# Kernel tuning notes

Measured on AMD Instinct MI355X. Metric: run time of the kernel, lower is better.

## Reference

```python
import jax, jax.numpy as jnp
import numpy as np

K = 16  # neighbors

def setup_inputs() -> dict:
    key = jax.random.key(0)
    x = jax.random.normal(key, (2, 8192, 64), dtype=jnp.float32)
    return {"x": x}

def reference(x):
    # pairwise squared euclidean distance: ||xi||^2 - 2 xi.xj + ||xj||^2
    b, n, d = x.shape
    x_inner = -2.0 * jnp.einsum('bnd,bmd->bnm', x, x)          # (B,N,N)
    x_sq = jnp.sum(x * x, axis=-1, keepdims=True)               # (B,N,1)
    dist = x_sq + x_inner + jnp.swapaxes(x_sq, 1, 2)            # (B,N,N)
    # torch.topk(-dist, k) -> largest of -dist == k nearest neighbors
    _, nn_idx = jax.lax.top_k(-dist, K)                         # (B,N,K) int32
    center_idx = jnp.broadcast_to(jnp.arange(n, dtype=nn_idx.dtype)[None, :, None], (b, n, K))
    return jnp.stack((nn_idx, center_idx), axis=0)              # (2,B,N,K)
```

## Files before the change

### kernel.cpp

```cpp
#include <hip/hip_runtime.h>
#include <stdint.h>

constexpr int N_   = 8192;
constexpr int D_   = 64;
constexpr int K_   = 16;
constexpr int NQ   = 16384;
constexpr int MS   = 8;
constexpr int CAPB = 32;
constexpr float SLOP = 0.012f;

typedef __attribute__((ext_vector_type(8))) short bf16x8;
typedef __attribute__((ext_vector_type(4))) float f32x4;

template<int JN>
__device__ __forceinline__ void topk_insertf(float (&key)[JN], float nk) {
    if (nk < key[JN - 1]) {
        bool c[JN];
#pragma unroll
        for (int j = 0; j < JN; ++j) c[j] = nk < key[j];
#pragma unroll
        for (int j = JN - 1; j >= 1; --j)
            key[j] = c[j - 1] ? key[j - 1] : (c[j] ? nk : key[j]);
        key[0] = c[0] ? nk : key[0];
    }
}

__device__ __forceinline__ unsigned short bf16_rne(float f) {
    uint32_t u = __float_as_uint(f);
    return (unsigned short)((u + 0x7FFFu + ((u >> 16) & 1u)) >> 16);
}

__device__ __forceinline__ void gl_lds16(const void* g, void* l) {
    __builtin_amdgcn_global_load_lds(
        (const __attribute__((address_space(1))) unsigned int*)g,
        (__attribute__((address_space(3))) unsigned int*)l, 16, 0, 0);
}

#define SWZ(r, s) (((r) << 7) + ((((s) ^ ((r) & 7))) << 4))

__global__ void __launch_bounds__(256) split_k(const float* __restrict__ x,
                                               unsigned short* __restrict__ xh,
                                               unsigned short* __restrict__ xl,
                                               float* __restrict__ nrm) {
    const int t = blockIdx.x * 256 + (int)threadIdx.x;
    const int row = t >> 4, seg = t & 15;
    const float4 v = reinterpret_cast<const float4*>(x)[t];
    float f[4] = {v.x, v.y, v.z, v.w};
    unsigned short h[4], l[4];
    float sq = 0.f;
#pragma unroll
    for (int j = 0; j < 4; ++j) {
        sq = fmaf(f[j], f[j], sq);
        h[j] = bf16_rne(f[j]);
        float hf = __uint_as_float((uint32_t)h[j] << 16);
        l[j] = bf16_rne(f[j] - hf);
    }
    sq += __shfl_xor(sq, 1, 16); sq += __shfl_xor(sq, 2, 16);
    sq += __shfl_xor(sq, 4, 16); sq += __shfl_xor(sq, 8, 16);
    if (seg == 0) nrm[row] = sq;
    ushort4 hv = {h[0], h[1], h[2], h[3]}, lv = {l[0], l[1], l[2], l[3]};
    reinterpret_cast<ushort4*>(xh)[t] = hv;
    reinterpret_cast<ushort4*>(xl)[t] = lv;
}

__global__ void __launch_bounds__(256) tau_p(const unsigned short* __restrict__ xh,
                                             const unsigned short* __restrict__ xl,
                                             const float* __restrict__ nrm,
                                             float* __restrict__ part) {
    __shared__ alignas(16) unsigned short A[64 * 64];
    __shared__ alignas(16) unsigned short Bb[256 * 64];
    __shared__ float nrmb[128];
    const int tid = (int)threadIdx.x;
    const int q0g = (int)blockIdx.x * 32;
    const int b   = q0g >> 13;
    const int n0  = q0g & (N_ - 1);
    const unsigned short* __restrict__ xhb = xh + (size_t)b * N_ * D_;
    const unsigned short* __restrict__ xlb = xl + (size_t)b * N_ * D_;
    const float* __restrict__ nb = nrm + b * N_;

#pragma unroll
    for (int k = 0; k < 2; ++k) {
        int u = tid + k * 256, r = u >> 3, s = u & 7;
        const unsigned short* src = (r < 32) ? xhb + (size_t)(n0 + r) * D_
                                             : xlb + (size_t)(n0 + r - 32) * D_;
        *(float4*)((char*)A + SWZ(r, s)) = *(const float4*)((const char*)src + (s << 4));
    }

    const int wave = tid >> 6, lane = tid & 63;
    const int l15 = lane & 15, quad = lane >> 4;

    float lad0[8], lad1[8];
#pragma unroll
    for (int j = 0; j < 8; ++j) { lad0[j] = __builtin_inff(); lad1[j] = __builtin_inff(); }

    for (int mc = 0; mc < 16; ++mc) {
        const int m0 = mc * 128;
        __syncthreads();
#pragma unroll
        for (int k = 0; k < 8; ++k) {
            int u = tid + k * 256, r = u >> 3, s = u & 7;
            const unsigned short* src = (r < 128) ? xhb + (size_t)(m0 + r) * D_
                                                  : xlb + (size_t)(m0 + r - 128) * D_;
            *(float4*)((char*)Bb + SWZ(r, s)) = *(const float4*)((const char*)src + (s << 4));
        }
        if (tid < 128) nrmb[tid] = nb[m0 + tid];
        __syncthreads();

        f32x4 acc[2][2] = {};
#pragma unroll
        for (int half = 0; half < 2; ++half) {
            const int seg = half * 4 + quad;
            bf16x8 afh[2], afl[2], bfh[2], bfl[2];
#pragma unroll
            for (int tm = 0; tm < 2; ++tm) {
                afh[tm] = *(const bf16x8*)((const char*)A + SWZ(tm * 16 + l15, seg));
                afl[tm] = *(const bf16x8*)((const char*)A + SWZ(32 + tm * 16 + l15, seg));
            }
#pragma unroll
            for (int tn = 0; tn < 2; ++tn) {
                bfh[tn] = *(const bf16x8*)((const char*)Bb + SWZ(wave * 32 + tn * 16 + l15, seg));
                bfl[tn] = *(const bf16x8*)((const char*)Bb + SWZ(128 + wave * 32 + tn * 16 + l15, seg));
            }
#pragma unroll
            for (int tm = 0; tm < 2; ++tm)
#pragma unroll
                for (int tn = 0; tn < 2; ++tn) {
                    acc[tm][tn] = __builtin_amdgcn_mfma_f32_16x16x32_bf16(afh[tm], bfh[tn], acc[tm][tn], 0, 0, 0);
                    acc[tm][tn] = __builtin_amdgcn_mfma_f32_16x16x32_bf16(afh[tm], bfl[tn], acc[tm][tn], 0, 0, 0);
                    acc[tm][tn] = __builtin_amdgcn_mfma_f32_16x16x32_bf16(afl[tm], bfh[tn], acc[tm][tn], 0, 0, 0);
                }
        }
#pragma unroll
        for (int tn = 0; tn < 2; ++tn) {
            const float nm = nrmb[wave * 32 + tn * 16 + l15];
#pragma unroll
            for (int tm = 0; tm < 2; ++tm)
#pragma unroll
                for (int reg = 0; reg < 4; ++reg) {
                    float keyf = fmaf(-2.f, acc[tm][tn][reg], nm);
                    const int li = tm * 4 + reg;
                    float k0 = lad0[li];
                    lad0[li] = fminf(k0, keyf);
                    lad1[li] = fminf(fmaxf(keyf, k0), lad1[li]);
                }
        }
    }
#pragma unroll
    for (int tm = 0; tm < 2; ++tm)
#pragma unroll
        for (int reg = 0; reg < 4; ++reg) {
            const int r = tm * 16 + quad * 4 + reg;
            const int li = tm * 4 + reg;
            float2 v = {lad0[li], lad1[li]};
            *(float2*)(part + ((size_t)(q0g + r)) * 128 + (wave * 16 + l15) * 2) = v;
        }
}

__global__ void __launch_bounds__(64) tau_m(const float* __restrict__ part,
                                            float* __restrict__ tau) {
    const int q = blockIdx.x * 64 + (int)threadIdx.x;
    const float4* p = reinterpret_cast<const float4*>(part + (size_t)q * 128);
    float key[K_];
#pragma unroll
    for (int j = 0; j < K_; ++j) key[j] = __builtin_inff();
    for (int i = 0; i < 32; ++i) {
        float4 v = p[i];
        topk_insertf<K_>(key, v.x); topk_insertf<K_>(key, v.y);
        topk_insertf<K_>(key, v.z); topk_insertf<K_>(key, v.w);
    }
    tau[q] = key[15] + SLOP;
}

__global__ void __launch_bounds__(256, 2) filter_k(const unsigned short* __restrict__ xh,
                                                   const unsigned short* __restrict__ xl,
                                                   const float* __restrict__ nrm,
                                                   const float* __restrict__ tau,
                                                   unsigned short* __restrict__ cnt_pb,
                                                   unsigned short* __restrict__ buf2) {
    __shared__ alignas(16) unsigned short A[256 * 64];
    __shared__ alignas(16) unsigned short Bd[2][128 * 64];
    __shared__ alignas(16) float taub[128];
    __shared__ alignas(16) float nrmS[1024];
    __shared__ unsigned short lists[128 * CAPB];
    __shared__ unsigned int cntL[128];
    const int tid = (int)threadIdx.x;
    const int bid = (int)blockIdx.x;
    const int b  = bid >> 9;
    const int qt = (bid >> 3) & 63;
    const int ms = bid & 7;
    const int q0 = qt * 128;
    const unsigned short* __restrict__ xhb = xh + (size_t)b * N_ * D_;
    const unsigned short* __restrict__ xlb = xl + (size_t)b * N_ * D_;
    const float* __restrict__ nb = nrm + b * N_;
    const int w = tid >> 6;

#pragma unroll
    for (int k = 0; k < 8; ++k) {
        int u = k * 256 + tid, r = u >> 3, sg = (u & 7) ^ (r & 7);
        const unsigned short* src = (r < 128) ? xhb + (size_t)(q0 + r) * D_
                                              : xlb + (size_t)(q0 + r - 128) * D_;
        gl_lds16((const char*)src + (sg << 4), (char*)A + (k << 12) + (w << 10));
    }
    {
        const int m0 = ms * 1024;
#pragma unroll
        for (int k = 0; k < 4; ++k) {
            int u = k * 256 + tid, r = u >> 3, sg = (u & 7) ^ (r & 7);
            const unsigned short* src = (r < 64) ? xhb + (size_t)(m0 + r) * D_
                                                 : xlb + (size_t)(m0 + r - 64) * D_;
            gl_lds16((const char*)src + (sg << 4), (char*)Bd[0] + (k << 12) + (w << 10));
        }
    }
    *(float4*)(nrmS + tid * 4) = *(const float4*)(nb + ms * 1024 + tid * 4);
    if (tid < 128) { cntL[tid] = 0; taub[tid] = tau[(b << 13) + q0 + tid]; }
    __syncthreads();

    const int lane = tid & 63;
    const int wq = w >> 1, wm = w & 1;
    const int l15 = lane & 15, quad = lane >> 4;

    bf16x8 Afh[2][4], Afl[2][4];
#pragma unroll
    for (int half = 0; half < 2; ++half) {
        const int seg = half * 4 + quad;
#pragma unroll
        for (int tm = 0; tm < 4; ++tm) {
            Afh[half][tm] = *(const bf16x8*)((const char*)A + SWZ(wq * 64 + tm * 16 + l15, seg));
            Afl[half][tm] = *(const bf16x8*)((const char*)A + SWZ(128 + wq * 64 + tm * 16 + l15, seg));
        }
    }
    f32x4 t4v[4];
#pragma unroll
    for (int tm = 0; tm < 4; ++tm)
        t4v[tm] = *(const f32x4*)(taub + wq * 64 + tm * 16 + quad * 4) + SLOP;

    for (int mc = 0; mc < 16; ++mc) {
        const int cur = mc & 1;
        if (mc < 15) {
            const int m0n = ms * 1024 + (mc + 1) * 64;
#pragma unroll
            for (int k = 0; k < 4; ++k) {
                int u = k * 256 + tid, r = u >> 3, sg = (u & 7) ^ (r & 7);
                const unsigned short* src = (r < 64) ? xhb + (size_t)(m0n + r) * D_
                                                     : xlb + (size_t)(m0n + r - 64) * D_;
                gl_lds16((const char*)src + (sg << 4), (char*)Bd[1 - cur] + (k << 12) + (w << 10));
            }
        }

        f32x4 acc[4][2] = {};
#pragma unroll
        for (int half = 0; half < 2; ++half) {
            const int seg = half * 4 + quad;
            bf16x8 bfh[2], bfl[2];
#pragma unroll
            for (int tn = 0; tn < 2; ++tn) {
                bfh[tn] = *(const bf16x8*)((const char*)Bd[cur] + SWZ(wm * 32 + tn * 16 + l15, seg));
                bfl[tn] = *(const bf16x8*)((const char*)Bd[cur] + SWZ(64 + wm * 32 + tn * 16 + l15, seg));
            }
#pragma unroll
            for (int tm = 0; tm < 4; ++tm)
#pragma unroll
                for (int tn = 0; tn < 2; ++tn) {
                    acc[tm][tn] = __builtin_amdgcn_mfma_f32_16x16x32_bf16(Afh[half][tm], bfh[tn], acc[tm][tn], 0, 0, 0);
                    acc[tm][tn] = __builtin_amdgcn_mfma_f32_16x16x32_bf16(Afh[half][tm], bfl[tn], acc[tm][tn], 0, 0, 0);
                    acc[tm][tn] = __builtin_amdgcn_mfma_f32_16x16x32_bf16(Afl[half][tm], bfh[tn], acc[tm][tn], 0, 0, 0);
                }
        }

        float nmv[2]; int mlv[2];
#pragma unroll
        for (int tn = 0; tn < 2; ++tn) {
            mlv[tn] = mc * 64 + wm * 32 + tn * 16 + l15;
            nmv[tn] = nrmS[mlv[tn]];
        }
#pragma unroll
        for (int tm = 0; tm < 4; ++tm)
#pragma unroll
            for (int tn = 0; tn < 2; ++tn)
#pragma unroll
                for (int reg = 0; reg < 4; ++reg) {
                    float keyf = fmaf(-2.f, acc[tm][tn][reg], nmv[tn]);
                    if (keyf <= t4v[tm][reg]) {
                        int ql = wq * 64 + tm * 16 + quad * 4 + reg;
                        unsigned pos = atomicAdd(&cntL[ql], 1u);
                        if (pos < CAPB) lists[ql * CAPB + pos] = (unsigned short)(ms * 1024 + mlv[tn]);
                    }
                }

        __syncthreads();
    }
    if (tid < 128) {
        int q = (b << 13) + q0 + tid;
        unsigned cn = cntL[tid]; cn = cn < CAPB ? cn : CAPB;
        cnt_pb[(size_t)q * MS + ms] = (unsigned short)cn;
        unsigned short* dst = buf2 + ((size_t)q * MS + ms) * CAPB;
        for (unsigned i = 0; i < cn; ++i) dst[i] = lists[tid * CAPB + i];
    }
}

__global__ void __launch_bounds__(256) rerank_k(const float* __restrict__ x,
                                                const unsigned short* __restrict__ cnt_pb,
                                                const unsigned short* __restrict__ buf2,
                                                int* __restrict__ out) {
    __shared__ float Qs[4 * 64];
    __shared__ unsigned short ids[4 * MS * CAPB];
    const int tid = (int)threadIdx.x;
    const int w = tid >> 6, lane = tid & 63;
    const int q = blockIdx.x * 4 + w;
    const int b = q >> 13, n = q & (N_ - 1);
    const float* __restrict__ xb = x + (size_t)b * N_ * D_;
    Qs[w * 64 + lane] = xb[(size_t)n * D_ + lane];

    int off[MS + 1]; off[0] = 0;
#pragma unroll
    for (int ms = 0; ms < MS; ++ms) {
        int c = (int)cnt_pb[(size_t)q * MS + ms]; c = c < CAPB ? c : CAPB;
        off[ms + 1] = off[ms] + c;
    }
    const int total = off[MS];
    for (int idx = lane; idx < total; idx += 64) {
        int ms = 0;
#pragma unroll
        for (int t = 1; t < MS; ++t) ms += (idx >= off[t]) ? 1 : 0;
        ids[(w * MS) * CAPB + idx] = buf2[((size_t)q * MS + ms) * CAPB + (idx - off[ms])];
    }
    __syncthreads();

    unsigned long long v = ~0ull;
    int consumed = 0;
    bool first = true;
    while (first || consumed < total) {
        const int myIdx = first ? lane : consumed + lane - 16;
        const bool take = (first || lane >= 16) && myIdx < total;
        unsigned long long nk = ~0ull;
        if (take) {
            const int id = (int)ids[(w * MS) * CAPB + myIdx];
            const float* __restrict__ crow = xb + (size_t)id * D_;
            double a0 = 0.0, a1 = 0.0, a2 = 0.0, a3 = 0.0;
#pragma unroll
            for (int j = 0; j < 16; ++j) {
                const float4 c  = *(const float4*)(crow + j * 4);
                const float4 qv = *(const float4*)(Qs + w * 64 + j * 4);
                double d0 = (double)qv.x - (double)c.x; a0 = fma(d0, d0, a0);
                double d1 = (double)qv.y - (double)c.y; a1 = fma(d1, d1, a1);
                double d2 = (double)qv.z - (double)c.z; a2 = fma(d2, d2, a2);
                double d3 = (double)qv.w - (double)c.w; a3 = fma(d3, d3, a3);
            }
            double s = (a0 + a1) + (a2 + a3);
            nk = ((unsigned long long)__double_as_longlong(s) & ~0x1FFFull) | (unsigned)id;
        }
        if (first || lane >= 16) v = nk;
#pragma unroll
        for (int k = 2; k <= 64; k <<= 1)
#pragma unroll
            for (int j = k >> 1; j > 0; j >>= 1) {
                unsigned long long o = __shfl_xor(v, j, 64);
                const bool keepmin = (((lane & k) == 0) == ((lane & j) == 0));
                unsigned long long mn = v < o ? v : o;
                unsigned long long mx = v < o ? o : v;
                v = keepmin ? mn : mx;
            }
        consumed += first ? 64 : 48;
        first = false;
    }
    if (lane < K_) {
        out[(size_t)q * K_ + lane]                   = (int)(v & 0x1FFFull);
        out[(size_t)NQ * K_ + (size_t)q * K_ + lane] = n;
    }
}

extern "C" void kernel_launch(void* const* d_in, const int* in_sizes, int n_in,
                              void* d_out, int out_size, void* d_ws, size_t ws_size,
                              hipStream_t stream) {
    const float* x = (const float*)d_in[0];
    int* out = (int*)d_out;
    char* ws = (char*)d_ws;
    float*          nrm    = (float*)ws;
    float*          tau    = (float*)(ws + (64 << 10));
    unsigned short* cnt_pb = (unsigned short*)(ws + (128 << 10));
    unsigned short* xh     = (unsigned short*)(ws + (1 << 20));
    unsigned short* xl     = (unsigned short*)(ws + (3 << 20));
    unsigned short* buf2   = (unsigned short*)(ws + (5 << 20));
    float*          part   = (float*)(ws + (5 << 20));

    hipLaunchKernelGGL(split_k,  dim3(1024), dim3(256), 0, stream, x, xh, xl, nrm);
    hipLaunchKernelGGL(tau_p,    dim3(512),  dim3(256), 0, stream, xh, xl, nrm, part);
    hipLaunchKernelGGL(tau_m,    dim3(256),  dim3(64),  0, stream, part, tau);
    hipLaunchKernelGGL(filter_k, dim3(1024), dim3(256), 0, stream, xh, xl, nrm, tau, cnt_pb, buf2);
    hipLaunchKernelGGL(rerank_k, dim3(4096), dim3(256), 0, stream, x, cnt_pb, buf2, out);
}
```

Baseline: 242.5 us.

## Keep query fragments in registers, ballot-compact filter lists, and split tau_p across shards

Result: slower. 267.8 us (+10.4%).

```diff
diff --git a/kernel.cpp b/kernel.cpp
--- a/kernel.cpp
+++ b/kernel.cpp
@@ -1,12 +1,13 @@
 #include <hip/hip_runtime.h>
 #include <stdint.h>
 
-constexpr int N_   = 8192;
-constexpr int D_   = 64;
-constexpr int K_   = 16;
-constexpr int NQ   = 16384;
-constexpr int MS   = 8;
-constexpr int CAPB = 32;
+constexpr int N_    = 8192;
+constexpr int D_    = 64;
+constexpr int K_    = 16;
+constexpr int NQ    = 16384;
+constexpr int MS    = 8;
+constexpr int CAP_H = 20;
+constexpr int CAPB  = 2 * CAP_H;
 constexpr float SLOP = 0.012f;
 
 typedef __attribute__((ext_vector_type(8))) short bf16x8;
@@ -63,96 +64,102 @@
     reinterpret_cast<ushort4*>(xl)[t] = lv;
 }
 
-__global__ void __launch_bounds__(256) tau_p(const unsigned short* __restrict__ xh,
-                                             const unsigned short* __restrict__ xl,
-                                             const float* __restrict__ nrm,
-                                             float* __restrict__ part) {
-    __shared__ alignas(16) unsigned short A[64 * 64];
-    __shared__ alignas(16) unsigned short Bb[256 * 64];
-    __shared__ float nrmb[128];
+__global__ void __launch_bounds__(256, 4) tau_p(const unsigned short* __restrict__ xh,
+                                                const unsigned short* __restrict__ xl,
+                                                const float* __restrict__ nrm,
+                                                float* __restrict__ part) {
+    __shared__ alignas(16) unsigned short Bd[2][128 * 64];
+    __shared__ alignas(16) float nrmS[512];
     const int tid = (int)threadIdx.x;
-    const int q0g = (int)blockIdx.x * 32;
+    const int bid = (int)blockIdx.x;
+    const int qb  = bid >> 2, sh = bid & 3;
+    const int q0g = qb * 64;
     const int b   = q0g >> 13;
-    const int n0  = q0g & (N_ - 1);
+    const int q0l = q0g & (N_ - 1);
+    const int s0  = sh * 512;
     const unsigned short* __restrict__ xhb = xh + (size_t)b * N_ * D_;
     const unsigned short* __restrict__ xlb = xl + (size_t)b * N_ * D_;
     const float* __restrict__ nb = nrm + b * N_;
-
-#pragma unroll
-    for (int k = 0; k < 2; ++k) {
-        int u = tid + k * 256, r = u >> 3, s = u & 7;
-        const unsigned short* src = (r < 32) ? xhb + (size_t)(n0 + r) * D_
-                                             : xlb + (size_t)(n0 + r - 32) * D_;
-        *(float4*)((char*)A + SWZ(r, s)) = *(const float4*)((const char*)src + (s << 4));
-    }
-
-    const int wave = tid >> 6, lane = tid & 63;
+    const int w = tid >> 6, lane = tid & 63;
+    const int wq = w >> 1, wm = w & 1;
     const int l15 = lane & 15, quad = lane >> 4;
 
-    float lad0[8], lad1[8];
-#pragma unroll
-    for (int j = 0; j < 8; ++j) { lad0[j] = __builtin_inff(); lad1[j] = __builtin_inff(); }
-
-    for (int mc = 0; mc < 16; ++mc) {
-        const int m0 = mc * 128;
-        __syncthreads();
-#pragma unroll
-        for (int k = 0; k < 8; ++k) {
-            int u = tid + k * 256, r = u >> 3, s = u & 7;
-            const unsigned short* src = (r < 128) ? xhb + (size_t)(m0 + r) * D_
-                                                  : xlb + (size_t)(m0 + r - 128) * D_;
-            *(float4*)((char*)Bb + SWZ(r, s)) = *(const float4*)((const char*)src + (s << 4));
-        }
-        if (tid < 128) nrmb[tid] = nb[m0 + tid];
-        __syncthreads();
-
+    bf16x8 Afh[2][2], Afl[2][2];
+#pragma unroll
+    for (int half = 0; half < 2; ++half) {
+        const int ko = (half * 4 + quad) << 4;
+#pragma unroll
+        for (int tm = 0; tm < 2; ++tm) {
+            const int r = q0l + wq * 32 + tm * 16 + l15;
+            Afh[half][tm] = *(const bf16x8*)((const char*)(xhb + (size_t)r * D_) + ko);
+            Afl[half][tm] = *(const bf16x8*)((const char*)(xlb + (size_t)r * D_) + ko);
+        }
+    }
+    {
+#pragma unroll
+        for (int k = 0; k < 4; ++k) {
+            int u = k * 256 + tid, r = u >> 3, sg = (u & 7) ^ (r & 7);
+            const unsigned short* src = (r < 64) ? xhb + (size_t)(s0 + r) * D_
+                                                 : xlb + (size_t)(s0 + r - 64) * D_;
+            gl_lds16((const char*)src + (sg << 4), (char*)Bd[0] + (k << 12) + (w << 10));
+        }
+    }
+    *(float2*)(nrmS + tid * 2) = *(const float2*)(nb + s0 + tid * 2);
+
+    float lad[8];
+#pragma unroll
+    for (int j = 0; j < 8; ++j) lad[j] = __builtin_inff();
+    __syncthreads();
+
+    for (int mc = 0; mc < 8; ++mc) {
+        const int cur = mc & 1;
+        if (mc < 7) {
+            const int m0n = s0 + (mc + 1) * 64;
+#pragma unroll
+            for (int k = 0; k < 4; ++k) {
+                int u = k * 256 + tid, r = u >> 3, sg = (u & 7) ^ (r & 7);
+                const unsigned short* src = (r < 64) ? xhb + (size_t)(m0n + r) * D_
+                                                     : xlb + (size_t)(m0n + r - 64) * D_;
+                gl_lds16((const char*)src + (sg << 4), (char*)Bd[1 - cur] + (k << 12) + (w << 10));
+            }
+        }
         f32x4 acc[2][2] = {};
 #pragma unroll
         for (int half = 0; half < 2; ++half) {
             const int seg = half * 4 + quad;
-            bf16x8 afh[2], afl[2], bfh[2], bfl[2];
-#pragma unroll
-            for (int tm = 0; tm < 2; ++tm) {
-                afh[tm] = *(const bf16x8*)((const char*)A + SWZ(tm * 16 + l15, seg));
-                afl[tm] = *(const bf16x8*)((const char*)A + SWZ(32 + tm * 16 + l15, seg));
-            }
+            bf16x8 bfh[2], bfl[2];
 #pragma unroll
             for (int tn = 0; tn < 2; ++tn) {
-                bfh[tn] = *(const bf16x8*)((const char*)Bb + SWZ(wave * 32 + tn * 16 + l15, seg));
-                bfl[tn] = *(const bf16x8*)((const char*)Bb + SWZ(128 + wave * 32 + tn * 16 + l15, seg));
+                bfh[tn] = *(const bf16x8*)((const char*)Bd[cur] + SWZ(wm * 32 + tn * 16 + l15, seg));
+                bfl[tn] = *(const bf16x8*)((const char*)Bd[cur] + SWZ(64 + wm * 32 + tn * 16 + l15, seg));
             }
 #pragma unroll
             for (int tm = 0; tm < 2; ++tm)
 #pragma unroll
                 for (int tn = 0; tn < 2; ++tn) {
-                    acc[tm][tn] = __builtin_amdgcn_mfma_f32_16x16x32_bf16(afh[tm], bfh[tn], acc[tm][tn], 0, 0, 0);
-                    acc[tm][tn] = __builtin_amdgcn_mfma_f32_16x16x32_bf16(afh[tm], bfl[tn], acc[tm][tn], 0, 0, 0);
-                    acc[tm][tn] = __builtin_amdgcn_mfma_f32_16x16x32_bf16(afl[tm], bfh[tn], acc[tm][tn], 0, 0, 0);
+                    acc[tm][tn] = __builtin_amdgcn_mfma_f32_16x16x32_bf16(Afh[half][tm], bfh[tn], acc[tm][tn], 0, 0, 0);
+                    acc[tm][tn] = __builtin_amdgcn_mfma_f32_16x16x32_bf16(Afh[half][tm], bfl[tn], acc[tm][tn], 0, 0, 0);
+                    acc[tm][tn] = __builtin_amdgcn_mfma_f32_16x16x32_bf16(Afl[half][tm], bfh[tn], acc[tm][tn], 0, 0, 0);
                 }
         }
 #pragma unroll
         for (int tn = 0; tn < 2; ++tn) {
-            const float nm = nrmb[wave * 32 + tn * 16 + l15];
+            const float nm = nrmS[mc * 64 + wm * 32 + tn * 16 + l15];
 #pragma unroll
             for (int tm = 0; tm < 2; ++tm)
 #pragma unroll
-                for (int reg = 0; reg < 4; ++reg) {
-                    float keyf = fmaf(-2.f, acc[tm][tn][reg], nm);
-                    const int li = tm * 4 + reg;
-                    float k0 = lad0[li];
-                    lad0[li] = fminf(k0, keyf);
-                    lad1[li] = fminf(fmaxf(keyf, k0), lad1[li]);
-                }
-        }
+                for (int reg = 0; reg < 4; ++reg)
+                    lad[tm * 4 + reg] = fminf(lad[tm * 4 + reg],
+                                              fmaf(-2.f, acc[tm][tn][reg], nm));
+        }
+        __syncthreads();
     }
 #pragma unroll
     for (int tm = 0; tm < 2; ++tm)
 #pragma unroll
         for (int reg = 0; reg < 4; ++reg) {
-            const int r = tm * 16 + quad * 4 + reg;
-            const int li = tm * 4 + reg;
-            float2 v = {lad0[li], lad1[li]};
-            *(float2*)(part + ((size_t)(q0g + r)) * 128 + (wave * 16 + l15) * 2) = v;
+            const int q = q0g + wq * 32 + tm * 16 + quad * 4 + reg;
+            part[(size_t)q * 128 + sh * 32 + wm * 16 + l15] = lad[tm * 4 + reg];
         }
 }
 
@@ -171,18 +178,16 @@
     tau[q] = key[15] + SLOP;
 }
 
-__global__ void __launch_bounds__(256, 2) filter_k(const unsigned short* __restrict__ xh,
+__global__ void __launch_bounds__(256, 3) filter_k(const unsigned short* __restrict__ xh,
                                                    const unsigned short* __restrict__ xl,
                                                    const float* __restrict__ nrm,
                                                    const float* __restrict__ tau,
                                                    unsigned short* __restrict__ cnt_pb,
                                                    unsigned short* __restrict__ buf2) {
-    __shared__ alignas(16) unsigned short A[256 * 64];
     __shared__ alignas(16) unsigned short Bd[2][128 * 64];
-    __shared__ alignas(16) float taub[128];
     __shared__ alignas(16) float nrmS[1024];
-    __shared__ unsigned short lists[128 * CAPB];
-    __shared__ unsigned int cntL[128];
+    __shared__ unsigned short lists[2][128][CAP_H];
+    __shared__ unsigned short cnt2[2][128];
     const int tid = (int)threadIdx.x;
     const int bid = (int)blockIdx.x;
     const int b  = bid >> 9;
@@ -192,15 +197,26 @@
     const unsigned short* __restrict__ xhb = xh + (size_t)b * N_ * D_;
     const unsigned short* __restrict__ xlb = xl + (size_t)b * N_ * D_;
     const float* __restrict__ nb = nrm + b * N_;
-    const int w = tid >> 6;
-
-#pragma unroll
-    for (int k = 0; k < 8; ++k) {
-        int u = k * 256 + tid, r = u >> 3, sg = (u & 7) ^ (r & 7);
-        const unsigned short* src = (r < 128) ? xhb + (size_t)(q0 + r) * D_
-                                              : xlb + (size_t)(q0 + r - 128) * D_;
-        gl_lds16((const char*)src + (sg << 4), (char*)A + (k << 12) + (w << 10));
-    }
+    const int w = tid >> 6, lane = tid & 63;
+    const int wq = w >> 1, wm = w & 1;
+    const int l15 = lane & 15, quad = lane >> 4;
+
+    bf16x8 Afh[2][4], Afl[2][4];
+#pragma unroll
+    for (int half = 0; half < 2; ++half) {
+        const int ko = (half * 4 + quad) << 4;
+#pragma unroll
+        for (int tm = 0; tm < 4; ++tm) {
+            const int r = q0 + wq * 64 + tm * 16 + l15;
+            Afh[half][tm] = *(const bf16x8*)((const char*)(xhb + (size_t)r * D_) + ko);
+            Afl[half][tm] = *(const bf16x8*)((const char*)(xlb + (size_t)r * D_) + ko);
+        }
+    }
+    f32x4 t4v[4];
+#pragma unroll
+    for (int tm = 0; tm < 4; ++tm)
+        t4v[tm] = *(const f32x4*)(tau + (b << 13) + q0 + wq * 64 + tm * 16 + quad * 4) + SLOP;
+
     {
         const int m0 = ms * 1024;
 #pragma unroll
@@ -212,27 +228,14 @@
         }
     }
     *(float4*)(nrmS + tid * 4) = *(const float4*)(nb + ms * 1024 + tid * 4);
-    if (tid < 128) { cntL[tid] = 0; taub[tid] = tau[(b << 13) + q0 + tid]; }
+    if (tid < 128) { cnt2[0][tid] = 0; cnt2[1][tid] = 0; }
+
+    const unsigned long long qmask = 0xFFFFull << (quad * 16);
+    const unsigned lowm = (1u << l15) - 1u;
+    int cq[16];
+#pragma unroll
+    for (int j = 0; j < 16; ++j) cq[j] = 0;
     __syncthreads();
-
-    const int lane = tid & 63;
-    const int wq = w >> 1, wm = w & 1;
-    const int l15 = lane & 15, quad = lane >> 4;
-
-    bf16x8 Afh[2][4], Afl[2][4];
-#pragma unroll
-    for (int half = 0; half < 2; ++half) {
-        const int seg = half * 4 + quad;
-#pragma unroll
-        for (int tm = 0; tm < 4; ++tm) {
-            Afh[half][tm] = *(const bf16x8*)((const char*)A + SWZ(wq * 64 + tm * 16 + l15, seg));
-            Afl[half][tm] = *(const bf16x8*)((const char*)A + SWZ(128 + wq * 64 + tm * 16 + l15, seg));
-        }
-    }
-    f32x4 t4v[4];
-#pragma unroll
-    for (int tm = 0; tm < 4; ++tm)
-        t4v[tm] = *(const f32x4*)(taub + wq * 64 + tm * 16 + quad * 4) + SLOP;
 
     for (int mc = 0; mc < 16; ++mc) {
         const int cur = mc & 1;
@@ -246,7 +249,6 @@
                 gl_lds16((const char*)src + (sg << 4), (char*)Bd[1 - cur] + (k << 12) + (w << 10));
             }
         }
-
         f32x4 acc[4][2] = {};
 #pragma unroll
         for (int half = 0; half < 2; ++half) {
@@ -266,35 +268,48 @@
                     acc[tm][tn] = __builtin_amdgcn_mfma_f32_16x16x32_bf16(Afl[half][tm], bfh[tn], acc[tm][tn], 0, 0, 0);
                 }
         }
-
-        float nmv[2]; int mlv[2];
 #pragma unroll
         for (int tn = 0; tn < 2; ++tn) {
-            mlv[tn] = mc * 64 + wm * 32 + tn * 16 + l15;
-            nmv[tn] = nrmS[mlv[tn]];
-        }
+            const int mloc = wm * 32 + tn * 16 + l15;
+            const float nm = nrmS[mc * 64 + mloc];
+            const unsigned short mid = (unsigned short)(ms * 1024 + mc * 64 + mloc);
+#pragma unroll
+            for (int tm = 0; tm < 4; ++tm)
+#pragma unroll
+                for (int reg = 0; reg < 4; ++reg) {
+                    const float keyf = fmaf(-2.f, acc[tm][tn][reg], nm);
+                    const bool pred = keyf <= t4v[tm][reg];
+                    const unsigned long long m64 = __ballot(pred);
+                    const unsigned mv = (unsigned)((m64 & qmask) >> (quad * 16));
+                    const int li = tm * 4 + reg;
+                    if (pred) {
+                        const int pos = cq[li] + __popc(mv & lowm);
+                        if (pos < CAP_H)
+                            lists[wm][wq * 64 + tm * 16 + quad * 4 + reg][pos] = mid;
+                    }
+                    cq[li] += __popc(mv);
+                }
+        }
+        __syncthreads();
+    }
+    if (l15 == 0) {
 #pragma unroll
         for (int tm = 0; tm < 4; ++tm)
 #pragma unroll
-            for (int tn = 0; tn < 2; ++tn)
-#pragma unroll
-                for (int reg = 0; reg < 4; ++reg) {
-                    float keyf = fmaf(-2.f, acc[tm][tn][reg], nmv[tn]);
-                    if (keyf <= t4v[tm][reg]) {
-                        int ql = wq * 64 + tm * 16 + quad * 4 + reg;
-                        unsigned pos = atomicAdd(&cntL[ql], 1u);
-                        if (pos < CAPB) lists[ql * CAPB + pos] = (unsigned short)(ms * 1024 + mlv[tn]);
-                    }
-                }
-
-        __syncthreads();
-    }
+            for (int reg = 0; reg < 4; ++reg) {
+                int c = cq[tm * 4 + reg];
+                cnt2[wm][wq * 64 + tm * 16 + quad * 4 + reg] =
+                    (unsigned short)(c < CAP_H ? c : CAP_H);
+            }
+    }
+    __syncthreads();
     if (tid < 128) {
-        int q = (b << 13) + q0 + tid;
-        unsigned cn = cntL[tid]; cn = cn < CAPB ? cn : CAPB;
-        cnt_pb[(size_t)q * MS + ms] = (unsigned short)cn;
+        const int q = (b << 13) + q0 + tid;
+        const int c0 = cnt2[0][tid], c1 = cnt2[1][tid];
+        cnt_pb[(size_t)q * MS + ms] = (unsigned short)(c0 + c1);
         unsigned short* dst = buf2 + ((size_t)q * MS + ms) * CAPB;
-        for (unsigned i = 0; i < cn; ++i) dst[i] = lists[tid * CAPB + i];
+        for (int i = 0; i < c0; ++i) dst[i] = lists[0][tid][i];
+        for (int i = 0; i < c1; ++i) dst[c0 + i] = lists[1][tid][i];
     }
 }
 
@@ -384,7 +399,7 @@
     float*          part   = (float*)(ws + (5 << 20));
 
     hipLaunchKernelGGL(split_k,  dim3(1024), dim3(256), 0, stream, x, xh, xl, nrm);
-    hipLaunchKernelGGL(tau_p,    dim3(512),  dim3(256), 0, stream, xh, xl, nrm, part);
+    hipLaunchKernelGGL(tau_p,    dim3(1024), dim3(256), 0, stream, xh, xl, nrm, part);
     hipLaunchKernelGGL(tau_m,    dim3(256),  dim3(64),  0, stream, part, tau);
     hipLaunchKernelGGL(filter_k, dim3(1024), dim3(256), 0, stream, xh, xl, nrm, tau, cnt_pb, buf2);
     hipLaunchKernelGGL(rerank_k, dim3(4096), dim3(256), 0, stream, x, cnt_pb, buf2, out);
```
